# Kernel optimization log

Measured on AMD Instinct MI355X. Metric: run time of the kernel, lower is better.

The kernel has to match this reference:

```python
import jax, jax.numpy as jnp
import numpy as np

N = 2048   # num_nodes
DIN = 8    # num_inputs
DC = 8     # comm_channels
DH = 32    # ch_q == dh == dk == FF
K = 2      # message-passing iterations (args.k)


def setup_inputs() -> dict:
    key = jax.random.key(0)
    ks = jax.random.split(key, 16)
    def w(k_, shape):
        return jax.random.normal(k_, shape, dtype=jnp.float32) * 0.05
    return dict(
        x=jax.random.normal(ks[0], (1, N, DIN), dtype=jnp.float32),
        comms=jnp.zeros((1, N, DC), jnp.float32),  # reset comm state
        adj=(jax.random.uniform(ks[1], (N, N)) < 0.01).astype(jnp.float32),
        dense=jax.random.uniform(ks[2], (N, N), dtype=jnp.float32),
        mask=jnp.ones((N,), jnp.float32),
        W_enc=w(ks[3], (DIN + DC, DH)), b_enc=jnp.zeros((DH,), jnp.float32),
        Wq=w(ks[4], (DH, DH)), bq=jnp.zeros((DH,), jnp.float32),
        Wk=w(ks[5], (DH, DH)), bk=jnp.zeros((DH,), jnp.float32),
        Wv=w(ks[6], (DH, DH)), bv=jnp.zeros((DH,), jnp.float32),
        W1=w(ks[7], (3, DH)), b1=jnp.zeros((DH,), jnp.float32),
        W2=w(ks[8], (DH, DH)), b2=jnp.zeros((DH,), jnp.float32),
        W3=w(ks[9], (DH, 1)), b3=jnp.zeros((1,), jnp.float32),
        W_dec=w(ks[10], (DH, 1)), b_dec=jnp.zeros((1,), jnp.float32),
        W_comm=w(ks[11], (DH, DC)), b_comm=jnp.zeros((DC,), jnp.float32),
        k=K,
    )


def _learned_distance(h, adj, dense, Wq, bq, Wk, bk, Wv, bv, W1, b1, W2, b2, W3, b3):
    # h: (N, DH). Torch builds x[i,j] = h[j], y[i,j] = h[i];
    # out[i,j] = q(h_j) . k(h_i)  ==  (K @ Q^T)[i, j]
    q = h @ Wq + bq        # (N, dk)
    kk = h @ Wk + bk       # (N, dk)
    v = h @ Wv + bv        # (N, dh)
    dots = kk @ q.T        # (N, N)
    feats = jnp.stack([dots, adj, dense], axis=-1)   # (N, N, 3)
    f = jax.nn.relu(feats @ W1 + b1)                 # (N, N, FF)
    f = jax.nn.relu(f @ W2 + b2)                     # (N, N, FF)
    logits = (f @ W3 + b3)[..., 0]                   # (N, N)
    focus = jax.nn.softmax(logits, axis=1)           # softmax over dim 1 (j)
    return focus @ v                                 # feature[i] = sum_j focus[i,j] v[j]


def reference(x, comms, adj, dense, mask, W_enc, b_enc, Wq, bq, Wk, bk, Wv, bv,
              W1, b1, W2, b2, W3, b3, W_dec, b_dec, W_comm, b_comm, k):
    inp = jnp.concatenate([x, comms], axis=-1)[0]    # (N, DIN+DC)
    h = inp @ W_enc + b_enc                          # encoding -> (N, ch_q)
    for _ in range(k):                               # k message-passing steps w/ residual
        h = _learned_distance(h, adj, dense, Wq, bq, Wk, bk, Wv, bv,
                              W1, b1, W2, b2, W3, b3) + h
    # comm_decoding is computed in the torch module (state update); it does not
    # feed the returned value: comms_out = tanh(h @ W_comm + b_comm)
    _ = jnp.tanh(h @ W_comm + b_comm)
    out = (h @ W_dec + b_dec)[:, 0]                  # decoding -> (N,)
    neg = jnp.where(mask == 0, -jnp.inf, 0.0).astype(out.dtype)
    return out + neg                                  # non-rl final_feature_process
```

## Files before the change

### kernel.cpp

```cpp
#include <hip/hip_runtime.h>
#include <hip/hip_bf16.h>
#include <hip/hip_fp16.h>
#include <math.h>

#define NN 2048

typedef _Float16 f16x8 __attribute__((ext_vector_type(8)));
typedef _Float16 h2    __attribute__((ext_vector_type(2)));
typedef float    f32x4 __attribute__((ext_vector_type(4)));
typedef float    f32x2 __attribute__((ext_vector_type(2)));

union H8 { h2 h[4]; f16x8 v; };

__device__ __forceinline__ h2 pkrtz(float a, float b){
  return __builtin_bit_cast(h2, __builtin_amdgcn_cvt_pkrtz(a, b));
}
__device__ __forceinline__ h2 hfma(h2 a, h2 b, h2 c){
  return __builtin_elementwise_fma(a, b, c);
}
__device__ __forceinline__ h2 hmax0(h2 a){
  h2 z = {(_Float16)0.f, (_Float16)0.f};
  return __builtin_elementwise_max(a, z);
}
__device__ __forceinline__ f32x2 pmax0f(f32x2 a){
  f32x2 z = {0.f, 0.f};
  return __builtin_elementwise_max(a, z);
}

#if __has_builtin(__builtin_amdgcn_permlane16_swap) && __has_builtin(__builtin_amdgcn_permlane32_swap)
#define HAVE_PERMLANE 1
__device__ __forceinline__ void pl16(float &x, float &y){
  auto r = __builtin_amdgcn_permlane16_swap(__builtin_bit_cast(unsigned, x),
                                            __builtin_bit_cast(unsigned, y), false, false);
  x = __builtin_bit_cast(float, (unsigned)r[0]);
  y = __builtin_bit_cast(float, (unsigned)r[1]);
}
__device__ __forceinline__ void pl32(float &x, float &y){
  auto r = __builtin_amdgcn_permlane32_swap(__builtin_bit_cast(unsigned, x),
                                            __builtin_bit_cast(unsigned, y), false, false);
  x = __builtin_bit_cast(float, (unsigned)r[0]);
  y = __builtin_bit_cast(float, (unsigned)r[1]);
}
__device__ __forceinline__ float redsum4g(float v){
  float a = v, b = v; pl16(a, b); float s = a + b;
  float c = s, d = s; pl32(c, d); return c + d;
}
__device__ __forceinline__ float redmax4g(float v){
  float a = v, b = v; pl16(a, b); float s = fmaxf(a, b);
  float c = s, d = s; pl32(c, d); return fmaxf(c, d);
}
#else
#define HAVE_PERMLANE 0
__device__ __forceinline__ float redsum4g(float v){
  v += __shfl_xor(v, 16, 64); v += __shfl_xor(v, 32, 64); return v;
}
__device__ __forceinline__ float redmax4g(float v){
  v = fmaxf(v, __shfl_xor(v, 16, 64)); v = fmaxf(v, __shfl_xor(v, 32, 64)); return v;
}
#endif

__global__ void k_encqkv(const float* __restrict__ x, const float* __restrict__ comms,
    const float* __restrict__ Wenc, const float* __restrict__ benc,
    const float* __restrict__ Wq, const float* __restrict__ bq,
    const float* __restrict__ Wk, const float* __restrict__ bk,
    const float* __restrict__ Wv, const float* __restrict__ bv,
    const float* __restrict__ W1, const float* __restrict__ b1,
    const float* __restrict__ W2, const float* __restrict__ W3,
    float* __restrict__ h, _Float16* __restrict__ qh, _Float16* __restrict__ kh,
    _Float16* __restrict__ vpk,
    _Float16* __restrict__ W1h, _Float16* __restrict__ b1h,
    _Float16* __restrict__ W2t, _Float16* __restrict__ W3h)
{
  int t = threadIdx.x, b = blockIdx.x;
  if (b == 0){
    if (t < 96) W1h[t] = (_Float16)W1[t];
    if (t < 32) b1h[t] = (_Float16)b1[t];
    if (t < 32) W3h[t] = (_Float16)W3[t];
    #pragma unroll
    for (int idx = t; idx < 1024; idx += 256){
      int r = idx >> 5, c1 = idx & 31;
      int rr = r & 15;
      int c2 = 8*(rr>>2) + (rr&3) + ((r >= 16) ? 4 : 0);
      W2t[idx] = (_Float16)W2[c1*32 + c2];
    }
  }
  int r = t >> 5, c = t & 31;
  int row = b*8 + r;
  float acc = benc[c];
  #pragma unroll
  for (int d=0; d<8; ++d) acc = fmaf(x[row*8+d],     Wenc[d*32+c],     acc);
  #pragma unroll
  for (int d=0; d<8; ++d) acc = fmaf(comms[row*8+d], Wenc[(8+d)*32+c], acc);
  __shared__ float hs[8][32];
  hs[r][c] = acc;
  h[row*32+c] = acc;
  __syncthreads();
  float aq=bq[c], ak=bk[c], av=bv[c];
  #pragma unroll 8
  for (int d=0; d<32; ++d){
    float hv = hs[r][d];
    aq = fmaf(hv, Wq[d*32+c], aq);
    ak = fmaf(hv, Wk[d*32+c], ak);
    av = fmaf(hv, Wv[d*32+c], av);
  }
  qh[row*32+c] = (_Float16)aq;
  kh[row*32+c] = (_Float16)ak;
  vpk[b*256 + c*8 + r] = (_Float16)av;
}

__launch_bounds__(256)
__global__ void k_logits(const _Float16* __restrict__ qh, const _Float16* __restrict__ kh,
    const float* __restrict__ adj, const float* __restrict__ dense,
    const _Float16* __restrict__ W1h, const _Float16* __restrict__ b1h,
    const _Float16* __restrict__ W2t, const _Float16* __restrict__ W3h,
    const float* __restrict__ b2, const float* __restrict__ b3,
    float* __restrict__ logits)
{
  int t = threadIdx.x;
  int wave = t >> 6;
  int l = t & 63;
  int lj = l & 15, g = l >> 4;
  int j0 = blockIdx.x * 64 + wave * 16;
  int i0 = blockIdx.y * 16;
  int c1b = 8*g;

  f16x8 af = *(const f16x8*)(kh + (i0+lj)*32 + c1b);
  f16x8 bq = *(const f16x8*)(qh + (j0+lj)*32 + c1b);
  f32x4 dacc = {0.f,0.f,0.f,0.f};
  dacc = __builtin_amdgcn_mfma_f32_16x16x32_f16(af, bq, dacc, 0, 0, 0);

  h2 dsh[16];
#if HAVE_PERMLANE
  #pragma unroll
  for (int r=0;r<4;++r){
    float a = dacc[r], b = dacc[r];
    pl16(a, b);
    float a0 = a, a1 = a; pl32(a0, a1);
    float b0 = b, b1 = b; pl32(b0, b1);
    dsh[r]    = pkrtz(a0, a0);
    dsh[4+r]  = pkrtz(b0, b0);
    dsh[8+r]  = pkrtz(a1, a1);
    dsh[12+r] = pkrtz(b1, b1);
  }
#else
  #pragma unroll
  for (int m=0;m<16;++m){
    float dv = __shfl(dacc[m & 3], ((m >> 2) << 4) + lj, 64);
    dsh[m] = pkrtz(dv, dv);
  }
#endif

  h2 w10[4], w11[4], w12[4], b1v[4];
  #pragma unroll
  for (int p=0;p<4;++p){
    w10[p] = ((const h2*)(W1h      + c1b))[p];
    w11[p] = ((const h2*)(W1h + 32 + c1b))[p];
    w12[p] = ((const h2*)(W1h + 64 + c1b))[p];
    b1v[p] = ((const h2*)(b1h      + c1b))[p];
  }
  f16x8 w2f0 = *(const f16x8*)(W2t + lj*32 + c1b);
  f16x8 w2f1 = *(const f16x8*)(W2t + (16+lj)*32 + c1b);
  f32x4 b2lo = *(const f32x4*)(b2 + 8*g);
  f32x4 b2hi = *(const f32x4*)(b2 + 8*g + 4);
  f16x8 w3f = {(_Float16)0.f,(_Float16)0.f,(_Float16)0.f,(_Float16)0.f,
               (_Float16)0.f,(_Float16)0.f,(_Float16)0.f,(_Float16)0.f};
  if (lj == 0) w3f = *(const f16x8*)(W3h + c1b);
  f32x4 c3 = {0.f,0.f,0.f,0.f};
  if (g == 0) c3[0] = b3[0];

  h2 adjh[16], denh[16];
  #pragma unroll
  for (int m=0;m<16;++m){
    float a_ = adj  [(i0+m)*NN + j0 + lj];
    float d_ = dense[(i0+m)*NN + j0 + lj];
    adjh[m] = pkrtz(a_, a_);
    denh[m] = pkrtz(d_, d_);
  }

  #pragma unroll
  for (int m=0;m<16;++m){
    H8 fr;
    #pragma unroll
    for (int p=0;p<4;++p)
      fr.h[p] = hmax0(hfma(dsh[m], w10[p], hfma(adjh[m], w11[p], hfma(denh[m], w12[p], b1v[p]))));
    f32x4 a0 = __builtin_amdgcn_mfma_f32_16x16x32_f16(w2f0, fr.v, b2lo, 0,0,0);
    f32x4 a1 = __builtin_amdgcn_mfma_f32_16x16x32_f16(w2f1, fr.v, b2hi, 0,0,0);
    f32x2 q01 = pmax0f((f32x2){a0[0], a0[1]});
    f32x2 q23 = pmax0f((f32x2){a0[2], a0[3]});
    f32x2 q45 = pmax0f((f32x2){a1[0], a1[1]});
    f32x2 q67 = pmax0f((f32x2){a1[2], a1[3]});
    H8 pr;
    pr.h[0] = pkrtz(q01[0], q01[1]);
    pr.h[1] = pkrtz(q23[0], q23[1]);
    pr.h[2] = pkrtz(q45[0], q45[1]);
    pr.h[3] = pkrtz(q67[0], q67[1]);
    f32x4 d3 = __builtin_amdgcn_mfma_f32_16x16x32_f16(w3f, pr.v, c3, 0,0,0);
    if (g == 0) logits[(i0+m)*NN + j0 + lj] = d3[0];
  }
}

template<int LAST>
__launch_bounds__(256)
__global__ void k_pv(const float* __restrict__ logits,
    const _Float16* __restrict__ vpk, const float* __restrict__ h_in,
    float* __restrict__ h_out,
    const float* __restrict__ Wq, const float* __restrict__ bq,
    const float* __restrict__ Wk, const float* __restrict__ bk,
    const float* __restrict__ Wv, const float* __restrict__ bv,
    _Float16* __restrict__ qn, _Float16* __restrict__ kn, _Float16* __restrict__ vpkn,
    const float* __restrict__ Wdec, const float* __restrict__ bdec,
    const float* __restrict__ mask, float* __restrict__ out)
{
  int t = threadIdx.x;
  int w = t >> 6;
  int l = t & 63;
  int li = l & 15, g = l >> 4;
  int i0 = blockIdx.x * 16;
  int jw = w * 512;
  const float* lrow = logits + (i0+li)*NN + jw + 8*g;

  f32x4 mx4 = {-INFINITY,-INFINITY,-INFINITY,-INFINITY};
  for (int s=0; s<16; ++s){
    f32x4 p0 = *(const f32x4*)(lrow + s*32);
    f32x4 p1 = *(const f32x4*)(lrow + s*32 + 4);
    #pragma unroll
    for (int e=0;e<4;++e){ mx4[e] = fmaxf(mx4[e], p0[e]); mx4[e] = fmaxf(mx4[e], p1[e]); }
  }
  float mxl = redmax4g(fmaxf(fmaxf(mx4[0],mx4[1]), fmaxf(mx4[2],mx4[3])));
  __shared__ float Ms[4][16];
  if (l < 16) Ms[w][l] = mxl;
  __syncthreads();
  float Mrow = fmaxf(fmaxf(Ms[0][li],Ms[1][li]), fmaxf(Ms[2][li],Ms[3][li]));

  f32x4 acc0 = {0.f,0.f,0.f,0.f}, acc1 = {0.f,0.f,0.f,0.f};
  float Lp = 0.f;
  for (int s=0; s<16; ++s){
    int jb = jw + s*32 + 8*g;
    f32x4 p0 = *(const f32x4*)(lrow + s*32);
    f32x4 p1 = *(const f32x4*)(lrow + s*32 + 4);
    float ex[8];
    #pragma unroll
    for (int e=0;e<4;++e){ ex[e] = __expf(p0[e] - Mrow); ex[4+e] = __expf(p1[e] - Mrow); }
    H8 pfr;
    #pragma unroll
    for (int p=0;p<4;++p) pfr.h[p] = pkrtz(ex[2*p], ex[2*p+1]);
    Lp += ((ex[0]+ex[1])+(ex[2]+ex[3])) + ((ex[4]+ex[5])+(ex[6]+ex[7]));
    int base = (jb >> 3) * 256;
    f16x8 vf0 = *(const f16x8*)(vpk + base + li*8);
    f16x8 vf1 = *(const f16x8*)(vpk + base + (16+li)*8);
    acc0 = __builtin_amdgcn_mfma_f32_16x16x32_f16(pfr.v, vf0, acc0, 0,0,0);
    acc1 = __builtin_amdgcn_mfma_f32_16x16x32_f16(pfr.v, vf1, acc1, 0,0,0);
  }
  Lp = redsum4g(Lp);
  __shared__ float accs[4][16][32];
  __shared__ float Ls[4][16];
  __shared__ float hsn[16][32];
  #pragma unroll
  for (int r=0;r<4;++r){
    accs[w][4*g+r][li]    = acc0[r];
    accs[w][4*g+r][16+li] = acc1[r];
  }
  if (l < 16) Ls[w][l] = Lp;
  __syncthreads();
  for (int o = t; o < 512; o += 256){
    int i = o >> 5, c = o & 31;
    float s4 = accs[0][i][c] + accs[1][i][c] + accs[2][i][c] + accs[3][i][c];
    float L4 = Ls[0][i] + Ls[1][i] + Ls[2][i] + Ls[3][i];
    float hnew = h_in[(i0+i)*32 + c] + s4 / L4;
    hsn[i][c] = hnew;
    if (!LAST) h_out[(i0+i)*32+c] = hnew;
  }
  __syncthreads();
  if (!LAST){
    for (int o = t; o < 512; o += 256){
      int i = o >> 5, c = o & 31;
      float aq = bq[c], ak = bk[c], av = bv[c];
      #pragma unroll 8
      for (int d=0; d<32; ++d){
        float hv = hsn[i][d];
        aq = fmaf(hv, Wq[d*32+c], aq);
        ak = fmaf(hv, Wk[d*32+c], ak);
        av = fmaf(hv, Wv[d*32+c], av);
      }
      int row = i0 + i;
      qn[row*32+c] = (_Float16)aq;
      kn[row*32+c] = (_Float16)ak;
      vpkn[(row>>3)*256 + c*8 + (row&7)] = (_Float16)av;
    }
  } else {
    __shared__ float red[16][16];
    int ii = t >> 4, cs = t & 15;
    float part = hsn[ii][2*cs]*Wdec[2*cs] + hsn[ii][2*cs+1]*Wdec[2*cs+1];
    red[ii][cs] = part;
    __syncthreads();
    if (t < 16){
      float sacc = 0.f;
      #pragma unroll
      for (int e=0;e<16;++e) sacc += red[t][e];
      float o = sacc + bdec[0];
      float mk = mask[i0+t];
      out[i0+t] = o + (mk == 0.f ? -INFINITY : 0.f);
    }
  }
}

extern "C" void kernel_launch(void* const* d_in, const int* in_sizes, int n_in,
                              void* d_out, int out_size, void* d_ws, size_t ws_size,
                              hipStream_t stream)
{
  const float* x     = (const float*)d_in[0];
  const float* comms = (const float*)d_in[1];
  const float* adj   = (const float*)d_in[2];
  const float* dense = (const float*)d_in[3];
  const float* mask  = (const float*)d_in[4];
  const float* Wenc  = (const float*)d_in[5];
  const float* benc  = (const float*)d_in[6];
  const float* Wq    = (const float*)d_in[7];
  const float* bq    = (const float*)d_in[8];
  const float* Wk    = (const float*)d_in[9];
  const float* bk    = (const float*)d_in[10];
  const float* Wv    = (const float*)d_in[11];
  const float* bv    = (const float*)d_in[12];
  const float* W1    = (const float*)d_in[13];
  const float* b1    = (const float*)d_in[14];
  const float* W2    = (const float*)d_in[15];
  const float* b2    = (const float*)d_in[16];
  const float* W3    = (const float*)d_in[17];
  const float* b3    = (const float*)d_in[18];
  const float* Wdec  = (const float*)d_in[19];
  const float* bdec  = (const float*)d_in[20];
  float* out = (float*)d_out;

  float* logits = (float*)d_ws;
  float* h1 = logits + (size_t)NN*NN;
  float* h2 = h1 + NN*32;
  _Float16* qh1  = (_Float16*)(h2 + NN*32);
  _Float16* kh1  = qh1 + (size_t)NN*32;
  _Float16* qh2  = kh1 + (size_t)NN*32;
  _Float16* kh2  = qh2 + (size_t)NN*32;
  _Float16* vpk1 = kh2 + (size_t)NN*32;
  _Float16* vpk2 = vpk1 + (size_t)NN*32;
  _Float16* W1h  = vpk2 + (size_t)NN*32;
  _Float16* b1h  = W1h + 96;
  _Float16* W2t  = b1h + 32;
  _Float16* W3h  = W2t + 1024;

  k_encqkv<<<256, 256, 0, stream>>>(x, comms, Wenc, benc, Wq,bq,Wk,bk,Wv,bv,
                                    W1, b1, W2, W3,
                                    h1, qh1, kh1, vpk1, W1h, b1h, W2t, W3h);
  dim3 gl(32, 128);
  k_logits<<<gl, 256, 0, stream>>>(qh1, kh1, adj, dense, W1h, b1h, W2t, W3h,
                                   b2, b3, logits);
  k_pv<0><<<128, 256, 0, stream>>>(logits, vpk1, h1, h2,
                                   Wq,bq,Wk,bk,Wv,bv, qh2,kh2,vpk2,
                                   nullptr, nullptr, nullptr, nullptr);
  k_logits<<<gl, 256, 0, stream>>>(qh2, kh2, adj, dense, W1h, b1h, W2t, W3h,
                                   b2, b3, logits);
  k_pv<1><<<128, 256, 0, stream>>>(logits, vpk2, h2, nullptr,
                                   nullptr,nullptr,nullptr,nullptr,nullptr,nullptr,
                                   nullptr,nullptr,nullptr,
                                   Wdec, bdec, mask, out);
}
```

Measured before the change: 96.97 us.

## Process two j-tiles per wave in logits; halve rows per softmax-PV block

The logits kernel now has each wave handle two 16-column j tiles, sharing the K fragment and weight registers and interleaving independent MFMA chains for more ILP. The grid halves in x. The PV kernel now handles 8 rows per block instead of 16, with half the lanes masked to zero, which doubles the block count to 256 so more CUs have work. The cost is higher register pressure in the logits kernel and wasted MFMA lanes in the PV kernel.

After: 105.2 us. 1.08x slower.

```diff
diff --git a/kernel.cpp b/kernel.cpp
--- a/kernel.cpp
+++ b/kernel.cpp
@@ -120,33 +120,49 @@
   int wave = t >> 6;
   int l = t & 63;
   int lj = l & 15, g = l >> 4;
-  int j0 = blockIdx.x * 64 + wave * 16;
+  int j0 = blockIdx.x * 128 + wave * 32;
   int i0 = blockIdx.y * 16;
   int c1b = 8*g;
 
-  f16x8 af = *(const f16x8*)(kh + (i0+lj)*32 + c1b);
-  f16x8 bq = *(const f16x8*)(qh + (j0+lj)*32 + c1b);
-  f32x4 dacc = {0.f,0.f,0.f,0.f};
-  dacc = __builtin_amdgcn_mfma_f32_16x16x32_f16(af, bq, dacc, 0, 0, 0);
-
-  h2 dsh[16];
+  f16x8 af  = *(const f16x8*)(kh + (i0+lj)*32 + c1b);
+  f16x8 bqA = *(const f16x8*)(qh + (j0+lj)*32 + c1b);
+  f16x8 bqB = *(const f16x8*)(qh + (j0+16+lj)*32 + c1b);
+  f32x4 zc = {0.f,0.f,0.f,0.f};
+  f32x4 daccA = __builtin_amdgcn_mfma_f32_16x16x32_f16(af, bqA, zc, 0,0,0);
+  f32x4 daccB = __builtin_amdgcn_mfma_f32_16x16x32_f16(af, bqB, zc, 0,0,0);
+
+  h2 dshA[16], dshB[16];
 #if HAVE_PERMLANE
   #pragma unroll
   for (int r=0;r<4;++r){
-    float a = dacc[r], b = dacc[r];
-    pl16(a, b);
-    float a0 = a, a1 = a; pl32(a0, a1);
-    float b0 = b, b1 = b; pl32(b0, b1);
-    dsh[r]    = pkrtz(a0, a0);
-    dsh[4+r]  = pkrtz(b0, b0);
-    dsh[8+r]  = pkrtz(a1, a1);
-    dsh[12+r] = pkrtz(b1, b1);
+    {
+      float a = daccA[r], b = daccA[r];
+      pl16(a, b);
+      float a0 = a, a1 = a; pl32(a0, a1);
+      float b0 = b, b1 = b; pl32(b0, b1);
+      dshA[r]    = pkrtz(a0, a0);
+      dshA[4+r]  = pkrtz(b0, b0);
+      dshA[8+r]  = pkrtz(a1, a1);
+      dshA[12+r] = pkrtz(b1, b1);
+    }
+    {
+      float a = daccB[r], b = daccB[r];
+      pl16(a, b);
+      float a0 = a, a1 = a; pl32(a0, a1);
+      float b0 = b, b1 = b; pl32(b0, b1);
+      dshB[r]    = pkrtz(a0, a0);
+      dshB[4+r]  = pkrtz(b0, b0);
+      dshB[8+r]  = pkrtz(a1, a1);
+      dshB[12+r] = pkrtz(b1, b1);
+    }
   }
 #else
   #pragma unroll
   for (int m=0;m<16;++m){
-    float dv = __shfl(dacc[m & 3], ((m >> 2) << 4) + lj, 64);
-    dsh[m] = pkrtz(dv, dv);
+    float dA = __shfl(daccA[m & 3], ((m >> 2) << 4) + lj, 64);
+    float dB = __shfl(daccB[m & 3], ((m >> 2) << 4) + lj, 64);
+    dshA[m] = pkrtz(dA, dA);
+    dshB[m] = pkrtz(dB, dB);
   }
 #endif
 
@@ -168,34 +184,48 @@
   f32x4 c3 = {0.f,0.f,0.f,0.f};
   if (g == 0) c3[0] = b3[0];
 
-  h2 adjh[16], denh[16];
+  h2 adjA[16], denA[16], adjB[16], denB[16];
   #pragma unroll
   for (int m=0;m<16;++m){
-    float a_ = adj  [(i0+m)*NN + j0 + lj];
-    float d_ = dense[(i0+m)*NN + j0 + lj];
-    adjh[m] = pkrtz(a_, a_);
-    denh[m] = pkrtz(d_, d_);
+    const float* arow = adj   + (i0+m)*NN + j0 + lj;
+    const float* drow = dense + (i0+m)*NN + j0 + lj;
+    float aA = arow[0], aB = arow[16];
+    float dA = drow[0], dB = drow[16];
+    adjA[m] = pkrtz(aA, aA); adjB[m] = pkrtz(aB, aB);
+    denA[m] = pkrtz(dA, dA); denB[m] = pkrtz(dB, dB);
   }
 
   #pragma unroll
   for (int m=0;m<16;++m){
-    H8 fr;
+    H8 frA, frB;
     #pragma unroll
-    for (int p=0;p<4;++p)
-      fr.h[p] = hmax0(hfma(dsh[m], w10[p], hfma(adjh[m], w11[p], hfma(denh[m], w12[p], b1v[p]))));
-    f32x4 a0 = __builtin_amdgcn_mfma_f32_16x16x32_f16(w2f0, fr.v, b2lo, 0,0,0);
-    f32x4 a1 = __builtin_amdgcn_mfma_f32_16x16x32_f16(w2f1, fr.v, b2hi, 0,0,0);
-    f32x2 q01 = pmax0f((f32x2){a0[0], a0[1]});
-    f32x2 q23 = pmax0f((f32x2){a0[2], a0[3]});
-    f32x2 q45 = pmax0f((f32x2){a1[0], a1[1]});
-    f32x2 q67 = pmax0f((f32x2){a1[2], a1[3]});
-    H8 pr;
-    pr.h[0] = pkrtz(q01[0], q01[1]);
-    pr.h[1] = pkrtz(q23[0], q23[1]);
-    pr.h[2] = pkrtz(q45[0], q45[1]);
-    pr.h[3] = pkrtz(q67[0], q67[1]);
-    f32x4 d3 = __builtin_amdgcn_mfma_f32_16x16x32_f16(w3f, pr.v, c3, 0,0,0);
-    if (g == 0) logits[(i0+m)*NN + j0 + lj] = d3[0];
+    for (int p=0;p<4;++p){
+      frA.h[p] = hmax0(hfma(dshA[m], w10[p], hfma(adjA[m], w11[p], hfma(denA[m], w12[p], b1v[p]))));
+      frB.h[p] = hmax0(hfma(dshB[m], w10[p], hfma(adjB[m], w11[p], hfma(denB[m], w12[p], b1v[p]))));
+    }
+    f32x4 a0A = __builtin_amdgcn_mfma_f32_16x16x32_f16(w2f0, frA.v, b2lo, 0,0,0);
+    f32x4 a0B = __builtin_amdgcn_mfma_f32_16x16x32_f16(w2f0, frB.v, b2lo, 0,0,0);
+    f32x4 a1A = __builtin_amdgcn_mfma_f32_16x16x32_f16(w2f1, frA.v, b2hi, 0,0,0);
+    f32x4 a1B = __builtin_amdgcn_mfma_f32_16x16x32_f16(w2f1, frB.v, b2hi, 0,0,0);
+    f32x2 qA0 = pmax0f((f32x2){a0A[0], a0A[1]});
+    f32x2 qA1 = pmax0f((f32x2){a0A[2], a0A[3]});
+    f32x2 qA2 = pmax0f((f32x2){a1A[0], a1A[1]});
+    f32x2 qA3 = pmax0f((f32x2){a1A[2], a1A[3]});
+    f32x2 qB0 = pmax0f((f32x2){a0B[0], a0B[1]});
+    f32x2 qB1 = pmax0f((f32x2){a0B[2], a0B[3]});
+    f32x2 qB2 = pmax0f((f32x2){a1B[0], a1B[1]});
+    f32x2 qB3 = pmax0f((f32x2){a1B[2], a1B[3]});
+    H8 prA, prB;
+    prA.h[0] = pkrtz(qA0[0], qA0[1]); prA.h[1] = pkrtz(qA1[0], qA1[1]);
+    prA.h[2] = pkrtz(qA2[0], qA2[1]); prA.h[3] = pkrtz(qA3[0], qA3[1]);
+    prB.h[0] = pkrtz(qB0[0], qB0[1]); prB.h[1] = pkrtz(qB1[0], qB1[1]);
+    prB.h[2] = pkrtz(qB2[0], qB2[1]); prB.h[3] = pkrtz(qB3[0], qB3[1]);
+    f32x4 d3A = __builtin_amdgcn_mfma_f32_16x16x32_f16(w3f, prA.v, c3, 0,0,0);
+    f32x4 d3B = __builtin_amdgcn_mfma_f32_16x16x32_f16(w3f, prB.v, c3, 0,0,0);
+    if (g == 0){
+      logits[(i0+m)*NN + j0 + lj]      = d3A[0];
+      logits[(i0+m)*NN + j0 + 16 + lj] = d3B[0];
+    }
   }
 }
 
@@ -215,16 +245,19 @@
   int w = t >> 6;
   int l = t & 63;
   int li = l & 15, g = l >> 4;
-  int i0 = blockIdx.x * 16;
+  int i0 = blockIdx.x * 8;
+  bool act = (li < 8);
   int jw = w * 512;
-  const float* lrow = logits + (i0+li)*NN + jw + 8*g;
+  const float* lrow = logits + (i0 + (act ? li : 0))*NN + jw + 8*g;
 
   f32x4 mx4 = {-INFINITY,-INFINITY,-INFINITY,-INFINITY};
-  for (int s=0; s<16; ++s){
-    f32x4 p0 = *(const f32x4*)(lrow + s*32);
-    f32x4 p1 = *(const f32x4*)(lrow + s*32 + 4);
-    #pragma unroll
-    for (int e=0;e<4;++e){ mx4[e] = fmaxf(mx4[e], p0[e]); mx4[e] = fmaxf(mx4[e], p1[e]); }
+  if (act){
+    for (int s=0; s<16; ++s){
+      f32x4 p0 = *(const f32x4*)(lrow + s*32);
+      f32x4 p1 = *(const f32x4*)(lrow + s*32 + 4);
+      #pragma unroll
+      for (int e=0;e<4;++e){ mx4[e] = fmaxf(mx4[e], p0[e]); mx4[e] = fmaxf(mx4[e], p1[e]); }
+    }
   }
   float mxl = redmax4g(fmaxf(fmaxf(mx4[0],mx4[1]), fmaxf(mx4[2],mx4[3])));
   __shared__ float Ms[4][16];
@@ -236,11 +269,16 @@
   float Lp = 0.f;
   for (int s=0; s<16; ++s){
     int jb = jw + s*32 + 8*g;
-    f32x4 p0 = *(const f32x4*)(lrow + s*32);
-    f32x4 p1 = *(const f32x4*)(lrow + s*32 + 4);
     float ex[8];
-    #pragma unroll
-    for (int e=0;e<4;++e){ ex[e] = __expf(p0[e] - Mrow); ex[4+e] = __expf(p1[e] - Mrow); }
+    if (act){
+      f32x4 p0 = *(const f32x4*)(lrow + s*32);
+      f32x4 p1 = *(const f32x4*)(lrow + s*32 + 4);
+      #pragma unroll
+      for (int e=0;e<4;++e){ ex[e] = __expf(p0[e] - Mrow); ex[4+e] = __expf(p1[e] - Mrow); }
+    } else {
+      #pragma unroll
+      for (int e=0;e<8;++e) ex[e] = 0.f;
+    }
     H8 pfr;
     #pragma unroll
     for (int p=0;p<4;++p) pfr.h[p] = pkrtz(ex[2*p], ex[2*p+1]);
@@ -254,7 +292,7 @@
   Lp = redsum4g(Lp);
   __shared__ float accs[4][16][32];
   __shared__ float Ls[4][16];
-  __shared__ float hsn[16][32];
+  __shared__ float hsn[8][32];
   #pragma unroll
   for (int r=0;r<4;++r){
     accs[w][4*g+r][li]    = acc0[r];
@@ -262,8 +300,8 @@
   }
   if (l < 16) Ls[w][l] = Lp;
   __syncthreads();
-  for (int o = t; o < 512; o += 256){
-    int i = o >> 5, c = o & 31;
+  {
+    int i = t >> 5, c = t & 31;
     float s4 = accs[0][i][c] + accs[1][i][c] + accs[2][i][c] + accs[3][i][c];
     float L4 = Ls[0][i] + Ls[1][i] + Ls[2][i] + Ls[3][i];
     float hnew = h_in[(i0+i)*32 + c] + s4 / L4;
@@ -272,28 +310,27 @@
   }
   __syncthreads();
   if (!LAST){
-    for (int o = t; o < 512; o += 256){
-      int i = o >> 5, c = o & 31;
-      float aq = bq[c], ak = bk[c], av = bv[c];
-      #pragma unroll 8
-      for (int d=0; d<32; ++d){
-        float hv = hsn[i][d];
-        aq = fmaf(hv, Wq[d*32+c], aq);
-        ak = fmaf(hv, Wk[d*32+c], ak);
-        av = fmaf(hv, Wv[d*32+c], av);
-      }
-      int row = i0 + i;
-      qn[row*32+c] = (_Float16)aq;
-      kn[row*32+c] = (_Float16)ak;
-      vpkn[(row>>3)*256 + c*8 + (row&7)] = (_Float16)av;
-    }
+    int i = t >> 5, c = t & 31;
+    float aq = bq[c], ak = bk[c], av = bv[c];
+    #pragma unroll 8
+    for (int d=0; d<32; ++d){
+      float hv = hsn[i][d];
+      aq = fmaf(hv, Wq[d*32+c], aq);
+      ak = fmaf(hv, Wk[d*32+c], ak);
+      av = fmaf(hv, Wv[d*32+c], av);
+    }
+    int row = i0 + i;
+    qn[row*32+c] = (_Float16)aq;
+    kn[row*32+c] = (_Float16)ak;
+    vpkn[(row>>3)*256 + c*8 + (row&7)] = (_Float16)av;
   } else {
-    __shared__ float red[16][16];
+    __shared__ float red[8][16];
     int ii = t >> 4, cs = t & 15;
-    float part = hsn[ii][2*cs]*Wdec[2*cs] + hsn[ii][2*cs+1]*Wdec[2*cs+1];
-    red[ii][cs] = part;
+    if (ii < 8){
+      red[ii][cs] = hsn[ii][2*cs]*Wdec[2*cs] + hsn[ii][2*cs+1]*Wdec[2*cs+1];
+    }
     __syncthreads();
-    if (t < 16){
+    if (t < 8){
       float sacc = 0.f;
       #pragma unroll
       for (int e=0;e<16;++e) sacc += red[t][e];
@@ -348,15 +385,15 @@
   k_encqkv<<<256, 256, 0, stream>>>(x, comms, Wenc, benc, Wq,bq,Wk,bk,Wv,bv,
                                     W1, b1, W2, W3,
                                     h1, qh1, kh1, vpk1, W1h, b1h, W2t, W3h);
-  dim3 gl(32, 128);
+  dim3 gl(16, 128);
   k_logits<<<gl, 256, 0, stream>>>(qh1, kh1, adj, dense, W1h, b1h, W2t, W3h,
                                    b2, b3, logits);
-  k_pv<0><<<128, 256, 0, stream>>>(logits, vpk1, h1, h2,
+  k_pv<0><<<256, 256, 0, stream>>>(logits, vpk1, h1, h2,
                                    Wq,bq,Wk,bk,Wv,bv, qh2,kh2,vpk2,
                                    nullptr, nullptr, nullptr, nullptr);
   k_logits<<<gl, 256, 0, stream>>>(qh2, kh2, adj, dense, W1h, b1h, W2t, W3h,
                                    b2, b3, logits);
-  k_pv<1><<<128, 256, 0, stream>>>(logits, vpk2, h2, nullptr,
+  k_pv<1><<<256, 256, 0, stream>>>(logits, vpk2, h2, nullptr,
                                    nullptr,nullptr,nullptr,nullptr,nullptr,nullptr,
                                    nullptr,nullptr,nullptr,
                                    Wdec, bdec, mask, out);
```
